# Kernel optimization log

Hardware: AMD Instinct MI355X
Metric: run time of the kernel (lower is better)

The kernel has to match this reference:

```python
import jax, jax.numpy as jnp
import numpy as np

B, C, H, W = 8, 64, 256, 256
DW = 2 * C          # dw_channel
FFN = 2 * C         # ffn_channel
EPS = 1e-6


def setup_inputs() -> dict:
    key = jax.random.key(0)
    ks = jax.random.split(key, 16)
    f = lambda k, s, scale=1.0: (jax.random.normal(k, s, jnp.float32) * scale)
    return {
        "inp": f(ks[0], (B, C, H, W)),
        "w1": f(ks[1], (B, DW, C, 1, 1)),
        "b1": f(ks[2], (B, DW), 0.01),
        "w2": f(ks[3], (B, DW, 1, 3, 3)),
        "b2": f(ks[4], (B, DW), 0.01),
        "w3": f(ks[5], (B, C, DW // 2, 1, 1)),
        "b3": f(ks[6], (B, C), 0.01),
        "w4": f(ks[7], (B, FFN, C, 1, 1)),
        "b4": f(ks[8], (B, FFN), 0.01),
        "w5": f(ks[9], (B, C, FFN // 2, 1, 1)),
        "b5": f(ks[10], (B, C), 0.01),
        "ln1_w": jnp.ones((C,), jnp.float32),
        "ln1_b": jnp.zeros((C,), jnp.float32),
        "ln2_w": jnp.ones((C,), jnp.float32),
        "ln2_b": jnp.zeros((C,), jnp.float32),
        "sca_w": f(ks[11], (DW // 2, DW // 2, 1, 1), 0.05),
        "sca_b": jnp.zeros((DW // 2,), jnp.float32),
        "beta": f(ks[12], (1, C, 1, 1), 0.1),
        "gamma": f(ks[13], (1, C, 1, 1), 0.1),
    }


def _layernorm2d(x, w, b):
    # LayerNorm over channel dim per pixel (NAFNet LayerNorm2d)
    mu = jnp.mean(x, axis=1, keepdims=True)
    var = jnp.var(x, axis=1, keepdims=True)
    xn = (x - mu) * jax.lax.rsqrt(var + EPS)
    return xn * w[None, :, None, None] + b[None, :, None, None]


def _normalize_weights(w):
    # w: [B, co, ci, kh, kw]; Frobenius norm over (ci, kh, kw) per (b, co)
    nrm = jnp.sqrt(jnp.sum(w * w, axis=(2, 3, 4), keepdims=True))
    return w / nrm


def _pw(x, w, b):
    # per-sample 1x1 conv: x [B,ci,H,W], w [B,co,ci,1,1], b [B,co]
    return jnp.einsum("bchw,boc->bohw", x, w[:, :, :, 0, 0]) + b[:, :, None, None]


def _dw3x3(x, w, b):
    # per-sample depthwise 3x3: x [B,DW,H,W], w [B,DW,1,3,3], b [B,DW]
    def one(xi, wi):
        y = jax.lax.conv_general_dilated(
            xi[None], wi, window_strides=(1, 1), padding="SAME",
            dimension_numbers=("NCHW", "OIHW", "NCHW"),
            feature_group_count=DW)
        return y[0]
    return jax.vmap(one)(x, w) + b[:, :, None, None]


def _simple_gate(x):
    x1, x2 = jnp.split(x, 2, axis=1)
    return x1 * x2


def reference(inp, w1, b1, w2, b2, w3, b3, w4, b4, w5, b5,
              ln1_w, ln1_b, ln2_w, ln2_b, sca_w, sca_b, beta, gamma):
    x = _layernorm2d(inp, ln1_w, ln1_b)
    x = _pw(x, _normalize_weights(w1), b1)          # [B,DW,H,W]
    x = _dw3x3(x, _normalize_weights(w2), b2)       # [B,DW,H,W]
    x = _simple_gate(x)                             # [B,DW/2,H,W]
    pooled = jnp.mean(x, axis=(2, 3))               # [B,DW/2]
    sca = jnp.einsum("bc,oc->bo", pooled, sca_w[:, :, 0, 0]) + sca_b
    x = x * sca[:, :, None, None]
    x = _pw(x, _normalize_weights(w3), b3)          # [B,C,H,W]
    y = inp + x * beta
    x = _layernorm2d(y, ln2_w, ln2_b)
    x = _pw(x, _normalize_weights(w4), b4)          # [B,FFN,H,W]
    x = _simple_gate(x)                             # [B,FFN/2,H,W]
    x = _pw(x, _normalize_weights(w5), b5)          # [B,C,H,W]
    return y + x * gamma
```

## Files before the change

### kernel.cpp

```cpp
#include <hip/hip_runtime.h>
#include <hip/hip_bf16.h>

typedef __attribute__((ext_vector_type(8))) short short8;
typedef __attribute__((ext_vector_type(4))) float f32x4;

#define HWN 65536
#define WN 256
#define HN 256

#define W2N_OFF 0
#define W1BF_OFF 9216
#define W3BF_OFF 41984
#define W4BF_OFF 58368
#define W5BF_OFF 91136
#define POOL_OFF 107520
#define SCA_OFF 108032

static __device__ __forceinline__ short f2bs(float f) {
    union { __hip_bfloat16 h; short s; } u; u.h = __float2bfloat16(f); return u.s;
}
static __device__ __forceinline__ float bs2f(short s) {
    union { unsigned u; float f; } v; v.u = ((unsigned)(unsigned short)s) << 16; return v.f;
}

__device__ __forceinline__ void norm_row(const float* __restrict__ in,
                                         float* __restrict__ out, int n) {
    float s = 0.f;
    for (int i = 0; i < n; i++) { float v = in[i]; s += v * v; }
    float r = rsqrtf(s);
    for (int i = 0; i < n; i++) out[i] = in[i] * r;
}

__device__ __forceinline__ void norm_row_bf(const float* __restrict__ in,
                                            short* __restrict__ out, int n) {
    float s = 0.f;
    for (int i = 0; i < n; i++) { float v = in[i]; s += v * v; }
    float r = rsqrtf(s);
    for (int i = 0; i < n; i++) out[i] = f2bs(in[i] * r);
}

__global__ void k_prep(const float* __restrict__ w1, const float* __restrict__ w2,
                       const float* __restrict__ w3, const float* __restrict__ w4,
                       const float* __restrict__ w5, float* __restrict__ ws) {
    int r = blockIdx.x * 256 + threadIdx.x;
    short* w1bf = (short*)(ws + W1BF_OFF);
    short* w3bf = (short*)(ws + W3BF_OFF);
    short* w4bf = (short*)(ws + W4BF_OFF);
    short* w5bf = (short*)(ws + W5BF_OFF);
    if (r < 1024) {
        norm_row_bf(w1 + r * 64, w1bf + r * 64, 64);
    } else if (r < 2048) {
        int rr = r - 1024;
        norm_row(w2 + rr * 9, ws + W2N_OFF + rr * 9, 9);
    } else if (r < 2560) {
        int rr = r - 2048;
        norm_row_bf(w3 + rr * 64, w3bf + rr * 64, 64);
    } else if (r < 3584) {
        int rr = r - 2560;
        norm_row_bf(w4 + rr * 64, w4bf + rr * 64, 64);
    } else if (r < 4096) {
        int rr = r - 3584;
        norm_row_bf(w5 + rr * 64, w5bf + rr * 64, 64);
    }
}

__global__ __launch_bounds__(256, 3) void k1(
    const float* __restrict__ inp, const float* __restrict__ ln1w,
    const float* __restrict__ ln1b, const float* __restrict__ b1,
    const float* __restrict__ b2v, const float* __restrict__ ws,
    float* __restrict__ g) {
    const short* w1bf = (const short*)(ws + W1BF_OFF);
    const float* w2n = ws + W2N_OFF;
    const int b = blockIdx.x >> 8;
    const int tile = blockIdx.x & 255;
    const int x0 = (tile & 15) << 4, y0 = (tile >> 4) << 4;
    const int t = threadIdx.x;
    const int wave = t >> 6, lane = t & 63;
    const int n = lane & 15, q = lane >> 4;

    __shared__ short sP[2][324 * 24];

    float wc[16], bc[16];
#pragma unroll
    for (int j = 0; j < 8; j++) {
        wc[j] = ln1w[q * 8 + j];
        bc[j] = ln1b[q * 8 + j];
        wc[8 + j] = ln1w[32 + q * 8 + j];
        bc[8 + j] = ln1b[32 + q * 8 + j];
    }

    short8 afr0[6], afr1[6];
    const float* xb = inp + ((size_t)b << 22);
#pragma unroll
    for (int i = 0; i < 6; i++) {
        int mt = wave + i * 4;
        if (mt < 21) {
            int pix = mt * 16 + n;
            int hy = pix / 18, hx = pix - hy * 18;
            int yy = y0 - 1 + hy, xx = x0 - 1 + hx;
            bool inb = ((unsigned)yy < HN) && ((unsigned)xx < WN) && (pix < 324);
            const float* xin = xb + (yy * WN + xx);
            float x[16];
            float s = 0.f, s2 = 0.f;
#pragma unroll
            for (int j = 0; j < 8; j++) {
                float v0 = inb ? xin[(size_t)(q * 8 + j) << 16] : 0.f;
                float v1 = inb ? xin[(size_t)(32 + q * 8 + j) << 16] : 0.f;
                x[j] = v0; x[8 + j] = v1;
                s += v0 + v1; s2 += v0 * v0 + v1 * v1;
            }
            s += __shfl_xor(s, 16); s += __shfl_xor(s, 32);
            s2 += __shfl_xor(s2, 16); s2 += __shfl_xor(s2, 32);
            float mu = s * (1.f / 64.f);
            float var = s2 * (1.f / 64.f) - mu * mu;
            float rr = rsqrtf(var + 1e-6f);
            short8 a0, a1;
#pragma unroll
            for (int j = 0; j < 8; j++) {
                a0[j] = f2bs((x[j] - mu) * rr * wc[j] + bc[j]);
                a1[j] = f2bs((x[8 + j] - mu) * rr * wc[8 + j] + bc[8 + j]);
            }
            afr0[i] = a0; afr1[i] = a1;
        }
    }

    const short* w1b = w1bf + b * 128 * 64;
    const float* w2b = w2n + b * 128 * 9;
    const float* b1b = b1 + b * 128;
    const float* b2b = b2v + b * 128;
    const int lx = t & 15, ly = t >> 4;

    for (int cc = 0; cc < 8; cc++) {
        int outch = cc * 8 + (n < 8 ? n : 56 + n);
        short8 bf0 = *(const short8*)(w1b + outch * 64 + q * 8);
        short8 bf1 = *(const short8*)(w1b + outch * 64 + 32 + q * 8);
        float bias = b1b[outch];
        short* sp = sP[cc & 1];
#pragma unroll
        for (int i = 0; i < 6; i++) {
            int mt = wave + i * 4;
            if (mt < 21) {
                f32x4 d = {0.f, 0.f, 0.f, 0.f};
                d = __builtin_amdgcn_mfma_f32_16x16x32_bf16(afr0[i], bf0, d, 0, 0, 0);
                d = __builtin_amdgcn_mfma_f32_16x16x32_bf16(afr1[i], bf1, d, 0, 0, 0);
#pragma unroll
                for (int r = 0; r < 4; r++) {
                    int row = mt * 16 + q * 4 + r;
                    if (row < 324) sp[row * 24 + n] = f2bs(d[r] + bias);
                }
            }
        }
        __syncthreads();
        float accA[8], accB[8];
#pragma unroll
        for (int p = 0; p < 8; p++) {
            accA[p] = b2b[cc * 8 + p];
            accB[p] = b2b[64 + cc * 8 + p];
        }
#pragma unroll
        for (int ky = 0; ky < 3; ky++) {
#pragma unroll
            for (int kx = 0; kx < 3; kx++) {
                int yy = y0 + ly + ky - 1, xx = x0 + lx + kx - 1;
                bool valid = ((unsigned)yy < HN) && ((unsigned)xx < WN);
                int e = (ly + ky) * 18 + lx + kx;
                short8 pA = *(const short8*)&sp[e * 24];
                short8 pB = *(const short8*)&sp[e * 24 + 8];
#pragma unroll
                for (int p = 0; p < 8; p++) {
                    float va = valid ? bs2f(pA[p]) : 0.f;
                    float vb = valid ? bs2f(pB[p]) : 0.f;
                    accA[p] += va * w2b[(cc * 8 + p) * 9 + ky * 3 + kx];
                    accB[p] += vb * w2b[(64 + cc * 8 + p) * 9 + ky * 3 + kx];
                }
            }
        }
        size_t gbase = ((size_t)(b * 64 + cc * 8)) * HWN + (size_t)((y0 + ly) * WN + x0 + lx);
#pragma unroll
        for (int p = 0; p < 8; p++)
            g[gbase + ((size_t)p << 16)] = accA[p] * accB[p];
    }
}

__global__ __launch_bounds__(1024) void k_pool(const float* __restrict__ g,
                                               float* __restrict__ pooled) {
    int bc = blockIdx.x;
    const float* src = g + (size_t)bc * HWN;
    float s = 0.f;
    for (int i = threadIdx.x * 4; i < HWN; i += 4096) {
        f32x4 v = *(const f32x4*)&src[i];
        s += v[0] + v[1] + v[2] + v[3];
    }
    __shared__ float red[16];
    int lane = threadIdx.x & 63, wave = threadIdx.x >> 6;
#pragma unroll
    for (int off = 32; off; off >>= 1) s += __shfl_down(s, off);
    if (lane == 0) red[wave] = s;
    __syncthreads();
    if (threadIdx.x < 16) {
        float v = red[threadIdx.x];
#pragma unroll
        for (int off = 8; off; off >>= 1) v += __shfl_down(v, off);
        if (threadIdx.x == 0) pooled[bc] = v;
    }
}

__global__ void k_sca(const float* __restrict__ pooled,
                      const float* __restrict__ scaw,
                      const float* __restrict__ scab,
                      float* __restrict__ sca) {
    int t = threadIdx.x;
    int b = t >> 6, o = t & 63;
    float acc = scab[o];
    for (int c = 0; c < 64; c++)
        acc += pooled[b * 64 + c] * (1.f / 65536.f) * scaw[o * 64 + c];
    sca[t] = acc;
}

__global__ __launch_bounds__(256, 2) void k2(
    const float* __restrict__ inp, const float* g, const float* __restrict__ ws,
    const float* __restrict__ b3, const float* __restrict__ beta,
    const float* __restrict__ ln2w, const float* __restrict__ ln2b,
    const float* __restrict__ b4, const float* __restrict__ b5,
    const float* __restrict__ gamma, float* out) {
    const int b = blockIdx.x >> 9;
    const int px0 = (blockIdx.x & 511) << 7;
    const int t = threadIdx.x;
    const int wave = t >> 6, lane = t & 63;
    const int n = lane & 15, q = lane >> 4;

    __shared__ short sX[128 * 72];
    __shared__ short sY[64 * 136];
    __shared__ short sH[128 * 72];

    const float* scav = ws + SCA_OFF + b * 64;

    {
        const float* gb = g + ((size_t)b << 22) + px0;
        for (int i = t; i < 128 * 64; i += 256) {
            int c = i >> 7, px = i & 127;
            sX[px * 72 + c] = f2bs(gb[((size_t)c << 16) + px] * scav[c]);
        }
    }
    __syncthreads();

    {
        const short* w3b = (const short*)(ws + W3BF_OFF) + b * 64 * 64;
        const float* b3b = b3 + b * 64;
        for (int nc = 0; nc < 4; nc++) {
            int outch = nc * 16 + n;
            short8 bf0 = *(const short8*)(w3b + outch * 64 + q * 8);
            short8 bf1 = *(const short8*)(w3b + outch * 64 + 32 + q * 8);
            float b3v = b3b[outch], betav = beta[outch];
            const float* ib = inp + ((size_t)b << 22) + ((size_t)outch << 16) + px0;
            for (int mt = wave; mt < 8; mt += 4) {
                const short* arow = &sX[(mt * 16 + n) * 72];
                short8 a0 = *(const short8*)(arow + q * 8);
                short8 a1 = *(const short8*)(arow + 32 + q * 8);
                f32x4 d = {0.f, 0.f, 0.f, 0.f};
                d = __builtin_amdgcn_mfma_f32_16x16x32_bf16(a0, bf0, d, 0, 0, 0);
                d = __builtin_amdgcn_mfma_f32_16x16x32_bf16(a1, bf1, d, 0, 0, 0);
#pragma unroll
                for (int r = 0; r < 4; r++) {
                    int px = mt * 16 + q * 4 + r;
                    float y = ib[px] + betav * (d[r] + b3v);
                    sY[outch * 136 + px] = f2bs(y);
                }
            }
        }
    }
    __syncthreads();

    if (t < 128) {
        float s = 0.f, s2 = 0.f;
        for (int c = 0; c < 64; c++) {
            float v = bs2f(sY[c * 136 + t]);
            s += v; s2 += v * v;
        }
        float mu = s * (1.f / 64.f);
        float var = s2 * (1.f / 64.f) - mu * mu;
        float rr = rsqrtf(var + 1e-6f);
        for (int c = 0; c < 64; c++) {
            float xn = (bs2f(sY[c * 136 + t]) - mu) * rr * ln2w[c] + ln2b[c];
            sX[t * 72 + c] = f2bs(xn);
        }
    }
    __syncthreads();

    {
        const short* w4b = (const short*)(ws + W4BF_OFF) + b * 128 * 64;
        const float* b4b = b4 + b * 128;
        for (int cc = 0; cc < 8; cc++) {
            int outch = cc * 8 + (n < 8 ? n : 56 + n);
            short8 bf0 = *(const short8*)(w4b + outch * 64 + q * 8);
            short8 bf1 = *(const short8*)(w4b + outch * 64 + 32 + q * 8);
            float b4v = b4b[outch];
            for (int mt = wave; mt < 8; mt += 4) {
                const short* arow = &sX[(mt * 16 + n) * 72];
                short8 a0 = *(const short8*)(arow + q * 8);
                short8 a1 = *(const short8*)(arow + 32 + q * 8);
                f32x4 d = {0.f, 0.f, 0.f, 0.f};
                d = __builtin_amdgcn_mfma_f32_16x16x32_bf16(a0, bf0, d, 0, 0, 0);
                d = __builtin_amdgcn_mfma_f32_16x16x32_bf16(a1, bf1, d, 0, 0, 0);
#pragma unroll
                for (int r = 0; r < 4; r++) {
                    float val = d[r] + b4v;
                    float other = __shfl_xor(val, 8);
                    if (n < 8)
                        sH[(mt * 16 + q * 4 + r) * 72 + cc * 8 + n] = f2bs(val * other);
                }
            }
        }
    }
    __syncthreads();

    {
        const short* w5b = (const short*)(ws + W5BF_OFF) + b * 64 * 64;
        const float* b5b = b5 + b * 64;
        for (int nc = 0; nc < 4; nc++) {
            int outch = nc * 16 + n;
            short8 bf0 = *(const short8*)(w5b + outch * 64 + q * 8);
            short8 bf1 = *(const short8*)(w5b + outch * 64 + 32 + q * 8);
            float b5v = b5b[outch];
            for (int mt = wave; mt < 8; mt += 4) {
                const short* arow = &sH[(mt * 16 + n) * 72];
                short8 a0 = *(const short8*)(arow + q * 8);
                short8 a1 = *(const short8*)(arow + 32 + q * 8);
                f32x4 d = {0.f, 0.f, 0.f, 0.f};
                d = __builtin_amdgcn_mfma_f32_16x16x32_bf16(a0, bf0, d, 0, 0, 0);
                d = __builtin_amdgcn_mfma_f32_16x16x32_bf16(a1, bf1, d, 0, 0, 0);
#pragma unroll
                for (int r = 0; r < 4; r++)
                    sX[(mt * 16 + q * 4 + r) * 72 + outch] = f2bs(d[r] + b5v);
            }
        }
    }
    __syncthreads();

    {
        int px = t & 127, half = t >> 7;
        float* ob = out + ((size_t)b << 22) + px0;
        for (int c = half * 32; c < half * 32 + 32; c++) {
            float o = bs2f(sY[c * 136 + px]) + gamma[c] * bs2f(sX[px * 72 + c]);
            ob[((size_t)c << 16) + px] = o;
        }
    }
}

extern "C" void kernel_launch(void* const* d_in, const int* in_sizes, int n_in,
                              void* d_out, int out_size, void* d_ws, size_t ws_size,
                              hipStream_t stream) {
    const float* inp  = (const float*)d_in[0];
    const float* w1   = (const float*)d_in[1];
    const float* b1   = (const float*)d_in[2];
    const float* w2   = (const float*)d_in[3];
    const float* b2v  = (const float*)d_in[4];
    const float* w3   = (const float*)d_in[5];
    const float* b3   = (const float*)d_in[6];
    const float* w4   = (const float*)d_in[7];
    const float* b4   = (const float*)d_in[8];
    const float* w5   = (const float*)d_in[9];
    const float* b5   = (const float*)d_in[10];
    const float* ln1w = (const float*)d_in[11];
    const float* ln1b = (const float*)d_in[12];
    const float* ln2w = (const float*)d_in[13];
    const float* ln2b = (const float*)d_in[14];
    const float* scaw = (const float*)d_in[15];
    const float* scab = (const float*)d_in[16];
    const float* beta = (const float*)d_in[17];
    const float* gamma= (const float*)d_in[18];

    float* ws = (float*)d_ws;
    float* pooled = ws + POOL_OFF;
    float* sca = ws + SCA_OFF;
    float* g = (float*)d_out;
    float* out = (float*)d_out;

    k_prep<<<16, 256, 0, stream>>>(w1, w2, w3, w4, w5, ws);
    k1<<<2048, 256, 0, stream>>>(inp, ln1w, ln1b, b1, b2v, ws, g);
    k_pool<<<512, 1024, 0, stream>>>(g, pooled);
    k_sca<<<1, 512, 0, stream>>>(pooled, scaw, scab, sca);
    k2<<<4096, 256, 0, stream>>>(inp, g, ws, b3, beta, ln2w, ln2b, b4, b5,
                                 gamma, out);
}
```

Before: 632.8 us.

## Fuse pooling into k1 via atomics, keep residual in registers in k2

Removes the separate pooling kernel. k1 now reduces each gated tile with wave shuffles and shared memory, then atomically adds into a pooled buffer that k_prep zeroes. k1 also precomputes a validity mask so halo zero-padding is applied once when staging, and splits the staging buffer into two compact arrays. k2 keeps the residual y in registers instead of a shared tile, does LayerNorm with vectorised row reads, and writes the output directly with vector stores, dropping one shared buffer and one barrier. Occupancy hints are raised. This adds more register pressure and makes the pooled sum depend on atomic ordering, so it is not bitwise deterministic.

Result: faster. 593.2 us (-6.2%).

```diff
diff --git a/kernel.cpp b/kernel.cpp
--- a/kernel.cpp
+++ b/kernel.cpp
@@ -61,14 +61,16 @@
     } else if (r < 4096) {
         int rr = r - 3584;
         norm_row_bf(w5 + rr * 64, w5bf + rr * 64, 64);
-    }
-}
-
-__global__ __launch_bounds__(256, 3) void k1(
+    } else if (r < 4608) {
+        ws[POOL_OFF + (r - 4096)] = 0.f;
+    }
+}
+
+__global__ __launch_bounds__(256, 4) void k1(
     const float* __restrict__ inp, const float* __restrict__ ln1w,
     const float* __restrict__ ln1b, const float* __restrict__ b1,
     const float* __restrict__ b2v, const float* __restrict__ ws,
-    float* __restrict__ g) {
+    float* __restrict__ g, float* __restrict__ pooled) {
     const short* w1bf = (const short*)(ws + W1BF_OFF);
     const float* w2n = ws + W2N_OFF;
     const int b = blockIdx.x >> 8;
@@ -78,7 +80,9 @@
     const int wave = t >> 6, lane = t & 63;
     const int n = lane & 15, q = lane >> 4;
 
-    __shared__ short sP[2][324 * 24];
+    __shared__ short sPA[2][324 * 8];
+    __shared__ short sPB[2][324 * 8];
+    __shared__ float sRed[8 * 4 * 8];
 
     float wc[16], bc[16];
 #pragma unroll
@@ -124,6 +128,22 @@
         }
     }
 
+    unsigned vmask = 0;
+#pragma unroll
+    for (int i = 0; i < 6; i++) {
+        int mt = wave + i * 4;
+        if (mt < 21) {
+#pragma unroll
+            for (int r = 0; r < 4; r++) {
+                int row = mt * 16 + q * 4 + r;
+                int hy = row / 18, hx = row - hy * 18;
+                int yy = y0 - 1 + hy, xx = x0 - 1 + hx;
+                if (row < 324 && ((unsigned)yy < HN) && ((unsigned)xx < WN))
+                    vmask |= 1u << (i * 4 + r);
+            }
+        }
+    }
+
     const short* w1b = w1bf + b * 128 * 64;
     const float* w2b = w2n + b * 128 * 9;
     const float* b1b = b1 + b * 128;
@@ -135,7 +155,8 @@
         short8 bf0 = *(const short8*)(w1b + outch * 64 + q * 8);
         short8 bf1 = *(const short8*)(w1b + outch * 64 + 32 + q * 8);
         float bias = b1b[outch];
-        short* sp = sP[cc & 1];
+        short* spA = sPA[cc & 1];
+        short* spB = sPB[cc & 1];
 #pragma unroll
         for (int i = 0; i < 6; i++) {
             int mt = wave + i * 4;
@@ -146,7 +167,12 @@
 #pragma unroll
                 for (int r = 0; r < 4; r++) {
                     int row = mt * 16 + q * 4 + r;
-                    if (row < 324) sp[row * 24 + n] = f2bs(d[r] + bias);
+                    short val = ((vmask >> (i * 4 + r)) & 1u) ? f2bs(d[r] + bias)
+                                                              : (short)0;
+                    if (row < 324) {
+                        if (n < 8) spA[row * 8 + n] = val;
+                        else       spB[row * 8 + (n - 8)] = val;
+                    }
                 }
             }
         }
@@ -161,47 +187,38 @@
         for (int ky = 0; ky < 3; ky++) {
 #pragma unroll
             for (int kx = 0; kx < 3; kx++) {
-                int yy = y0 + ly + ky - 1, xx = x0 + lx + kx - 1;
-                bool valid = ((unsigned)yy < HN) && ((unsigned)xx < WN);
                 int e = (ly + ky) * 18 + lx + kx;
-                short8 pA = *(const short8*)&sp[e * 24];
-                short8 pB = *(const short8*)&sp[e * 24 + 8];
+                short8 pA = *(const short8*)&spA[e * 8];
+                short8 pB = *(const short8*)&spB[e * 8];
 #pragma unroll
                 for (int p = 0; p < 8; p++) {
-                    float va = valid ? bs2f(pA[p]) : 0.f;
-                    float vb = valid ? bs2f(pB[p]) : 0.f;
-                    accA[p] += va * w2b[(cc * 8 + p) * 9 + ky * 3 + kx];
-                    accB[p] += vb * w2b[(64 + cc * 8 + p) * 9 + ky * 3 + kx];
+                    accA[p] += bs2f(pA[p]) * w2b[(cc * 8 + p) * 9 + ky * 3 + kx];
+                    accB[p] += bs2f(pB[p]) * w2b[(64 + cc * 8 + p) * 9 + ky * 3 + kx];
                 }
             }
         }
+        float v[8];
         size_t gbase = ((size_t)(b * 64 + cc * 8)) * HWN + (size_t)((y0 + ly) * WN + x0 + lx);
 #pragma unroll
-        for (int p = 0; p < 8; p++)
-            g[gbase + ((size_t)p << 16)] = accA[p] * accB[p];
-    }
-}
-
-__global__ __launch_bounds__(1024) void k_pool(const float* __restrict__ g,
-                                               float* __restrict__ pooled) {
-    int bc = blockIdx.x;
-    const float* src = g + (size_t)bc * HWN;
-    float s = 0.f;
-    for (int i = threadIdx.x * 4; i < HWN; i += 4096) {
-        f32x4 v = *(const f32x4*)&src[i];
-        s += v[0] + v[1] + v[2] + v[3];
-    }
-    __shared__ float red[16];
-    int lane = threadIdx.x & 63, wave = threadIdx.x >> 6;
-#pragma unroll
-    for (int off = 32; off; off >>= 1) s += __shfl_down(s, off);
-    if (lane == 0) red[wave] = s;
+        for (int p = 0; p < 8; p++) {
+            v[p] = accA[p] * accB[p];
+            g[gbase + ((size_t)p << 16)] = v[p];
+        }
+#pragma unroll
+        for (int p = 0; p < 8; p++) {
+            float s = v[p];
+            s += __shfl_xor(s, 1);  s += __shfl_xor(s, 2);
+            s += __shfl_xor(s, 4);  s += __shfl_xor(s, 8);
+            s += __shfl_xor(s, 16); s += __shfl_xor(s, 32);
+            if (lane == 0) sRed[(cc * 4 + wave) * 8 + p] = s;
+        }
+    }
     __syncthreads();
-    if (threadIdx.x < 16) {
-        float v = red[threadIdx.x];
-#pragma unroll
-        for (int off = 8; off; off >>= 1) v += __shfl_down(v, off);
-        if (threadIdx.x == 0) pooled[bc] = v;
+    if (t < 64) {
+        int cc = t >> 3, p = t & 7;
+        float s = sRed[(cc * 4 + 0) * 8 + p] + sRed[(cc * 4 + 1) * 8 + p] +
+                  sRed[(cc * 4 + 2) * 8 + p] + sRed[(cc * 4 + 3) * 8 + p];
+        atomicAdd(&pooled[b * 64 + cc * 8 + p], s);
     }
 }
 
@@ -217,7 +234,7 @@
     sca[t] = acc;
 }
 
-__global__ __launch_bounds__(256, 2) void k2(
+__global__ __launch_bounds__(256, 4) void k2(
     const float* __restrict__ inp, const float* g, const float* __restrict__ ws,
     const float* __restrict__ b3, const float* __restrict__ beta,
     const float* __restrict__ ln2w, const float* __restrict__ ln2b,
@@ -230,8 +247,7 @@
     const int n = lane & 15, q = lane >> 4;
 
     __shared__ short sX[128 * 72];
-    __shared__ short sY[64 * 136];
-    __shared__ short sH[128 * 72];
+    __shared__ short sB[128 * 72];
 
     const float* scav = ws + SCA_OFF + b * 64;
 
@@ -244,45 +260,66 @@
     }
     __syncthreads();
 
+    float yreg[4][2][4];
     {
         const short* w3b = (const short*)(ws + W3BF_OFF) + b * 64 * 64;
         const float* b3b = b3 + b * 64;
+#pragma unroll
         for (int nc = 0; nc < 4; nc++) {
             int outch = nc * 16 + n;
             short8 bf0 = *(const short8*)(w3b + outch * 64 + q * 8);
             short8 bf1 = *(const short8*)(w3b + outch * 64 + 32 + q * 8);
             float b3v = b3b[outch], betav = beta[outch];
             const float* ib = inp + ((size_t)b << 22) + ((size_t)outch << 16) + px0;
-            for (int mt = wave; mt < 8; mt += 4) {
+#pragma unroll
+            for (int mi = 0; mi < 2; mi++) {
+                int mt = wave + mi * 4;
                 const short* arow = &sX[(mt * 16 + n) * 72];
                 short8 a0 = *(const short8*)(arow + q * 8);
                 short8 a1 = *(const short8*)(arow + 32 + q * 8);
                 f32x4 d = {0.f, 0.f, 0.f, 0.f};
                 d = __builtin_amdgcn_mfma_f32_16x16x32_bf16(a0, bf0, d, 0, 0, 0);
                 d = __builtin_amdgcn_mfma_f32_16x16x32_bf16(a1, bf1, d, 0, 0, 0);
+                f32x4 resid = *(const f32x4*)(ib + mt * 16 + q * 4);
 #pragma unroll
                 for (int r = 0; r < 4; r++) {
-                    int px = mt * 16 + q * 4 + r;
-                    float y = ib[px] + betav * (d[r] + b3v);
-                    sY[outch * 136 + px] = f2bs(y);
+                    float y = resid[r] + betav * (d[r] + b3v);
+                    yreg[nc][mi][r] = y;
+                    sB[(mt * 16 + q * 4 + r) * 72 + outch] = f2bs(y);
                 }
             }
         }
     }
     __syncthreads();
 
-    if (t < 128) {
+    {
+        int px = t >> 1, half = t & 1;
+        const short* yrow = &sB[px * 72 + half * 32];
+        short8 yv[4];
         float s = 0.f, s2 = 0.f;
-        for (int c = 0; c < 64; c++) {
-            float v = bs2f(sY[c * 136 + t]);
-            s += v; s2 += v * v;
-        }
+#pragma unroll
+        for (int v8 = 0; v8 < 4; v8++) {
+            yv[v8] = *(const short8*)(yrow + v8 * 8);
+#pragma unroll
+            for (int j = 0; j < 8; j++) {
+                float f = bs2f(yv[v8][j]);
+                s += f; s2 += f * f;
+            }
+        }
+        s += __shfl_xor(s, 1); s2 += __shfl_xor(s2, 1);
         float mu = s * (1.f / 64.f);
         float var = s2 * (1.f / 64.f) - mu * mu;
         float rr = rsqrtf(var + 1e-6f);
-        for (int c = 0; c < 64; c++) {
-            float xn = (bs2f(sY[c * 136 + t]) - mu) * rr * ln2w[c] + ln2b[c];
-            sX[t * 72 + c] = f2bs(xn);
+        short* xrow = &sX[px * 72 + half * 32];
+#pragma unroll
+        for (int v8 = 0; v8 < 4; v8++) {
+            short8 o;
+#pragma unroll
+            for (int j = 0; j < 8; j++) {
+                int c = half * 32 + v8 * 8 + j;
+                o[j] = f2bs((bs2f(yv[v8][j]) - mu) * rr * ln2w[c] + ln2b[c]);
+            }
+            *(short8*)(xrow + v8 * 8) = o;
         }
     }
     __syncthreads();
@@ -295,7 +332,9 @@
             short8 bf0 = *(const short8*)(w4b + outch * 64 + q * 8);
             short8 bf1 = *(const short8*)(w4b + outch * 64 + 32 + q * 8);
             float b4v = b4b[outch];
-            for (int mt = wave; mt < 8; mt += 4) {
+#pragma unroll
+            for (int mi = 0; mi < 2; mi++) {
+                int mt = wave + mi * 4;
                 const short* arow = &sX[(mt * 16 + n) * 72];
                 short8 a0 = *(const short8*)(arow + q * 8);
                 short8 a1 = *(const short8*)(arow + 32 + q * 8);
@@ -307,7 +346,7 @@
                     float val = d[r] + b4v;
                     float other = __shfl_xor(val, 8);
                     if (n < 8)
-                        sH[(mt * 16 + q * 4 + r) * 72 + cc * 8 + n] = f2bs(val * other);
+                        sB[(mt * 16 + q * 4 + r) * 72 + cc * 8 + n] = f2bs(val * other);
                 }
             }
         }
@@ -317,32 +356,28 @@
     {
         const short* w5b = (const short*)(ws + W5BF_OFF) + b * 64 * 64;
         const float* b5b = b5 + b * 64;
+        float* ob = out + ((size_t)b << 22) + px0;
+#pragma unroll
         for (int nc = 0; nc < 4; nc++) {
             int outch = nc * 16 + n;
             short8 bf0 = *(const short8*)(w5b + outch * 64 + q * 8);
             short8 bf1 = *(const short8*)(w5b + outch * 64 + 32 + q * 8);
-            float b5v = b5b[outch];
-            for (int mt = wave; mt < 8; mt += 4) {
-                const short* arow = &sH[(mt * 16 + n) * 72];
+            float b5v = b5b[outch], gam = gamma[outch];
+#pragma unroll
+            for (int mi = 0; mi < 2; mi++) {
+                int mt = wave + mi * 4;
+                const short* arow = &sB[(mt * 16 + n) * 72];
                 short8 a0 = *(const short8*)(arow + q * 8);
                 short8 a1 = *(const short8*)(arow + 32 + q * 8);
                 f32x4 d = {0.f, 0.f, 0.f, 0.f};
                 d = __builtin_amdgcn_mfma_f32_16x16x32_bf16(a0, bf0, d, 0, 0, 0);
                 d = __builtin_amdgcn_mfma_f32_16x16x32_bf16(a1, bf1, d, 0, 0, 0);
+                f32x4 o;
 #pragma unroll
                 for (int r = 0; r < 4; r++)
-                    sX[(mt * 16 + q * 4 + r) * 72 + outch] = f2bs(d[r] + b5v);
-            }
-        }
-    }
-    __syncthreads();
-
-    {
-        int px = t & 127, half = t >> 7;
-        float* ob = out + ((size_t)b << 22) + px0;
-        for (int c = half * 32; c < half * 32 + 32; c++) {
-            float o = bs2f(sY[c * 136 + px]) + gamma[c] * bs2f(sX[px * 72 + c]);
-            ob[((size_t)c << 16) + px] = o;
+                    o[r] = yreg[nc][mi][r] + gam * (d[r] + b5v);
+                *(f32x4*)(ob + ((size_t)outch << 16) + mt * 16 + q * 4) = o;
+            }
         }
     }
 }
@@ -376,9 +411,8 @@
     float* g = (float*)d_out;
     float* out = (float*)d_out;
 
-    k_prep<<<16, 256, 0, stream>>>(w1, w2, w3, w4, w5, ws);
-    k1<<<2048, 256, 0, stream>>>(inp, ln1w, ln1b, b1, b2v, ws, g);
-    k_pool<<<512, 1024, 0, stream>>>(g, pooled);
+    k_prep<<<17, 256, 0, stream>>>(w1, w2, w3, w4, w5, ws);
+    k1<<<2048, 256, 0, stream>>>(inp, ln1w, ln1b, b1, b2v, ws, g, pooled);
     k_sca<<<1, 512, 0, stream>>>(pooled, scaw, scab, sca);
     k2<<<4096, 256, 0, stream>>>(inp, g, ws, b3, beta, ln2w, ln2b, b4, b5,
                                  gamma, out);
```
